# Kernel optimization log

Measured on AMD Instinct MI355X. Metric: run time of the kernel, lower is better.

The kernel has to match this reference:

```python
import jax, jax.numpy as jnp
import numpy as np

T_LEN, BATCH, IN_SIZE, HID = 512, 64, 1024, 1024
EPS = 1e-6


def layer_norm(x, alpha, beta, eps=EPS):
    # Matches torch: mean over last dim, UNBIASED variance (ddof=1)
    mu = jnp.mean(x, axis=-1, keepdims=True)
    var = jnp.var(x, axis=-1, keepdims=True, ddof=1)
    xn = (x - mu) / jnp.sqrt(var + eps)
    return alpha * xn + beta


def setup_inputs() -> dict:
    key = jax.random.key(0)
    ks = jax.random.split(key, 12)
    std = 1.0 / np.sqrt(HID)
    u = lambda k, shape: jax.random.uniform(k, shape, jnp.float32, -std, std)
    return {
        "x": jax.random.normal(ks[0], (T_LEN, BATCH, IN_SIZE), jnp.float32),
        "Wi": u(ks[1], (4 * HID, IN_SIZE)),
        "bi": u(ks[2], (4 * HID,)),
        "Wh": u(ks[3], (4 * HID, HID)),
        "bh": u(ks[4], (4 * HID,)),
        "g_i2h": u(ks[5], (4 * HID,)),
        "b_i2h": u(ks[6], (4 * HID,)),
        "g_h2h": u(ks[7], (4 * HID,)),
        "b_h2h": u(ks[8], (4 * HID,)),
        "g_cell": u(ks[9], (HID,)),
        "b_cell": u(ks[10], (HID,)),
    }


def reference(x, Wi, bi, Wh, bh, g_i2h, b_i2h, g_h2h, b_h2h, g_cell, b_cell):
    # Faithful to the source: h and c are NEVER updated inside the loop
    # (the original code omits h = h_t / c = c_t), so every timestep sees
    # the initial zero state -> fully parallel over time.
    T, B, _ = x.shape
    H = Wh.shape[1]
    h0 = jnp.zeros((B, H), x.dtype)
    c0 = jnp.zeros((B, H), x.dtype)

    i2h = layer_norm(jnp.einsum('tbi,gi->tbg', x, Wi) + bi, g_i2h, b_i2h)  # [T,B,4H]
    h2h = layer_norm(h0 @ Wh.T + bh, g_h2h, b_h2h)                          # [B,4H]
    preact = i2h + h2h                                                      # [T,B,4H]

    gates = jax.nn.sigmoid(preact[..., :3 * H])
    g_t = jnp.tanh(preact[..., 3 * H:])
    f_t = gates[..., H:2 * H]
    o_t = gates[..., 2 * H:3 * H]
    # i_t = gates[..., :H] is computed in the original but unused

    c_t = c0 * f_t + (1.0 - f_t) * g_t
    c_t = layer_norm(c_t, g_cell, b_cell)
    h_t = o_t * jnp.tanh(c_t)  # [T,B,H]

    return h_t, h_t[-1]
```

## Files before the change

### kernel.cpp

```cpp
#include <hip/hip_runtime.h>
#include <hip/hip_bf16.h>
#include <stdint.h>


#define MROWS 32768L
#define NCOLS 4096
#define KDIM  1024

typedef __bf16 bf16x8 __attribute__((ext_vector_type(8)));
typedef __bf16 bf16x4 __attribute__((ext_vector_type(4)));
typedef float  f32x4  __attribute__((ext_vector_type(4)));

__device__ float g_Cvec[4096];

__device__ __forceinline__ void gload16(char* lds, const char* g) {
  __builtin_amdgcn_global_load_lds(
      (const __attribute__((address_space(1))) char*)g,
      (__attribute__((address_space(3))) char*)lds, 16, 0, 0);
}

__device__ __forceinline__ void block_reduce2(float& a, float& b, float* red, int tid) {
#pragma unroll
  for (int m = 32; m > 0; m >>= 1) {
    a += __shfl_xor(a, m, 64);
    b += __shfl_xor(b, m, 64);
  }
  const int lane = tid & 63, wid = tid >> 6;
  if (lane == 0) { red[wid] = a; red[4 + wid] = b; }
  __syncthreads();
  a = red[0] + red[1] + red[2] + red[3];
  b = red[4] + red[5] + red[6] + red[7];
  __syncthreads();
}

__global__ __launch_bounds__(256) void cast_kernel(const float4* __restrict__ in,
                                                   bf16x4* __restrict__ out, int n4) {
  int i = blockIdx.x * 256 + threadIdx.x;
  const int stride = gridDim.x * 256;
  for (; i < n4; i += stride) {
    const float4 v = in[i];
    bf16x4 o = { (__bf16)v.x, (__bf16)v.y, (__bf16)v.z, (__bf16)v.w };
    out[i] = o;
  }
}

__global__ __launch_bounds__(256) void prep_kernel(const float* __restrict__ bh,
                                                   const float* __restrict__ b_i2h,
                                                   const float* __restrict__ g_h2h,
                                                   const float* __restrict__ b_h2h) {
  __shared__ float red[8];
  const int tid = threadIdx.x;
  float v[16];
  float s = 0.f, ss = 0.f;
#pragma unroll
  for (int u = 0; u < 16; ++u) {
    v[u] = bh[tid + u * 256];
    s += v[u]; ss += v[u] * v[u];
  }
  block_reduce2(s, ss, red, tid);
  const float mu  = s * (1.f / 4096.f);
  const float var = (ss - 4096.f * mu * mu) * (1.f / 4095.f);
  const float rs  = rsqrtf(var + 1e-6f);
#pragma unroll
  for (int u = 0; u < 16; ++u) {
    const int g = tid + u * 256;
    g_Cvec[g] = b_i2h[g] + g_h2h[g] * ((v[u] - mu) * rs) + b_h2h[g];
  }
}

__global__ __launch_bounds__(256) void gemm_kernel(const __bf16* __restrict__ A,
                                                   const __bf16* __restrict__ B,
                                                   __bf16* __restrict__ Y, long r0) {
  __shared__ __align__(16) __bf16 As[128 * 64];
  __shared__ __align__(16) __bf16 Bs[128 * 64];
  const int tid  = threadIdx.x;
  const int lane = tid & 63;
  const int wid  = tid >> 6;
  const int wm   = wid >> 1;
  const int wn   = wid & 1;
  const int bid  = blockIdx.x;
  const long m0  = (long)(bid >> 5) * 128;
  const long n0  = (long)(bid & 31) * 128;

  const int srow  = tid >> 3;
  const int sbyte = (tid & 7) << 4;
  const char* Ag = (const char*)(A + (r0 + m0) * KDIM) + (long)srow * 2048 + sbyte;
  const char* Bg = (const char*)(B + n0 * KDIM) + (long)srow * 2048 + sbyte;
  char* Al = (char*)As + tid * 16;
  char* Bl = (char*)Bs + tid * 16;

  f32x4 acc[4][4];
  const f32x4 z = {0.f, 0.f, 0.f, 0.f};
#pragma unroll
  for (int i = 0; i < 4; ++i)
#pragma unroll
    for (int j = 0; j < 4; ++j) acc[i][j] = z;

  const int fr = lane & 15;
  const int fk = (lane >> 4) << 3;
  const __bf16* ArdBase = &As[(wm * 64 + fr) * 64 + fk];
  const __bf16* BrdBase = &Bs[(wn * 64 + fr) * 64 + fk];

  for (int kt = 0; kt < KDIM / 64; ++kt) {
    const long koff = (long)kt * 128;
#pragma unroll
    for (int c = 0; c < 4; ++c) {
      gload16(Al + c * 4096, Ag + (long)c * 32 * 2048 + koff);
      gload16(Bl + c * 4096, Bg + (long)c * 32 * 2048 + koff);
    }
    __syncthreads();
#pragma unroll
    for (int s = 0; s < 2; ++s) {
      bf16x8 a[4], b[4];
#pragma unroll
      for (int i = 0; i < 4; ++i) a[i] = *(const bf16x8*)(ArdBase + i * 16 * 64 + s * 32);
#pragma unroll
      for (int j = 0; j < 4; ++j) b[j] = *(const bf16x8*)(BrdBase + j * 16 * 64 + s * 32);
#pragma unroll
      for (int i = 0; i < 4; ++i)
#pragma unroll
        for (int j = 0; j < 4; ++j)
          acc[i][j] = __builtin_amdgcn_mfma_f32_16x16x32_bf16(a[i], b[j], acc[i][j], 0, 0, 0);
    }
    __syncthreads();
  }

  const long orow0 = m0 + wm * 64 + ((lane >> 4) << 2);
  const long ocol0 = n0 + wn * 64 + fr;
#pragma unroll
  for (int i = 0; i < 4; ++i)
#pragma unroll
    for (int j = 0; j < 4; ++j)
#pragma unroll
      for (int r = 0; r < 4; ++r)
        Y[(orow0 + i * 16 + r) * NCOLS + ocol0 + j * 16] = (__bf16)acc[i][j][r];
}

__global__ __launch_bounds__(256) void pass2_kernel(const __bf16* __restrict__ Yw,
                                                    const float* __restrict__ bi,
                                                    const float* __restrict__ g_i2h,
                                                    const float* __restrict__ g_cell,
                                                    const float* __restrict__ b_cell,
                                                    float* __restrict__ out, long r0) {
  __shared__ float p0[4096];
  __shared__ float red[8];
  const int tid  = threadIdx.x;
  const long row = r0 + blockIdx.x;
  const bf16x8* yv = (const bf16x8*)(Yw + (long)blockIdx.x * NCOLS);

  float s = 0.f, ss = 0.f;
#pragma unroll
  for (int it = 0; it < 2; ++it) {
    const int ch = tid + it * 256;
    const bf16x8 v = yv[ch];
    const float4 b0 = ((const float4*)bi)[ch * 2];
    const float4 b1 = ((const float4*)bi)[ch * 2 + 1];
    float p[8];
    p[0] = (float)v[0] + b0.x;  p[1] = (float)v[1] + b0.y;
    p[2] = (float)v[2] + b0.z;  p[3] = (float)v[3] + b0.w;
    p[4] = (float)v[4] + b1.x;  p[5] = (float)v[5] + b1.y;
    p[6] = (float)v[6] + b1.z;  p[7] = (float)v[7] + b1.w;
#pragma unroll
    for (int u = 0; u < 8; ++u) {
      p0[ch * 8 + u] = p[u];
      s += p[u];
      ss += p[u] * p[u];
    }
  }
  block_reduce2(s, ss, red, tid);
  const float mu  = s * (1.f / 4096.f);
  const float var = (ss - 4096.f * mu * mu) * (1.f / 4095.f);
  const float rs  = rsqrtf(var + 1e-6f);

  float cc[4], oo[4];
  float s2 = 0.f, ss2 = 0.f;
#pragma unroll
  for (int u = 0; u < 4; ++u) {
    const int j = tid + u * 256;
    const float pf = g_i2h[1024 + j] * ((p0[1024 + j] - mu) * rs) + g_Cvec[1024 + j];
    const float po = g_i2h[2048 + j] * ((p0[2048 + j] - mu) * rs) + g_Cvec[2048 + j];
    const float pg = g_i2h[3072 + j] * ((p0[3072 + j] - mu) * rs) + g_Cvec[3072 + j];
    const float f  = 1.f / (1.f + __expf(-pf));
    oo[u] = 1.f / (1.f + __expf(-po));
    const float e2 = __expf(2.f * pg);
    const float gt = (e2 - 1.f) / (e2 + 1.f);
    cc[u] = (1.f - f) * gt;
    s2 += cc[u]; ss2 += cc[u] * cc[u];
  }
  block_reduce2(s2, ss2, red, tid);
  const float mu2  = s2 * (1.f / 1024.f);
  const float var2 = (ss2 - 1024.f * mu2 * mu2) * (1.f / 1023.f);
  const float rs2  = rsqrtf(var2 + 1e-6f);

  const long obase = row * 1024;
#pragma unroll
  for (int u = 0; u < 4; ++u) {
    const int j = tid + u * 256;
    const float cn = g_cell[j] * ((cc[u] - mu2) * rs2) + b_cell[j];
    const float e2 = __expf(2.f * cn);
    const float th = (e2 - 1.f) / (e2 + 1.f);
    const float h  = oo[u] * th;
    out[obase + j] = h;
    if (row >= MROWS - 64)
      out[MROWS * 1024 + ((row - (MROWS - 64)) << 10) + j] = h;
  }
}

extern "C" void kernel_launch(void* const* d_in, const int* in_sizes, int n_in,
                              void* d_out, int out_size, void* d_ws, size_t ws_size,
                              hipStream_t stream) {
  (void)in_sizes; (void)n_in; (void)out_size;
  const float* x      = (const float*)d_in[0];
  const float* Wi     = (const float*)d_in[1];
  const float* bi     = (const float*)d_in[2];
  const float* bh     = (const float*)d_in[4];
  const float* g_i2h  = (const float*)d_in[5];
  const float* b_i2h  = (const float*)d_in[6];
  const float* g_h2h  = (const float*)d_in[7];
  const float* b_h2h  = (const float*)d_in[8];
  const float* g_cell = (const float*)d_in[9];
  const float* b_cell = (const float*)d_in[10];
  float* out = (float*)d_out;

  __bf16* xb = (__bf16*)d_out;
  __bf16* wb = (__bf16*)((char*)d_out + 67108864);
  __bf16* y  = (__bf16*)d_ws;

  cast_kernel<<<2048, 256, 0, stream>>>((const float4*)x, (bf16x4*)xb, 33554432 / 4);
  cast_kernel<<<1024, 256, 0, stream>>>((const float4*)Wi, (bf16x4*)wb, 4194304 / 4);
  prep_kernel<<<1, 256, 0, stream>>>(bh, b_i2h, g_h2h, b_h2h);

  long max_rows = (long)(ws_size / (NCOLS * 2)) & ~127L;
  if (max_rows > MROWS) max_rows = MROWS;
  if (max_rows < 128)   max_rows = 128;
  for (long rbase = 0; rbase < MROWS; rbase += max_rows) {
    const long rows = (MROWS - rbase < max_rows) ? (MROWS - rbase) : max_rows;
    gemm_kernel<<<dim3((rows / 128) * 32), 256, 0, stream>>>(xb, wb, y, rbase);
    pass2_kernel<<<dim3(rows), 256, 0, stream>>>(y, bi, g_i2h, g_cell, b_cell, out, rbase);
  }
}
```

Measured before the change: 501.0 us.

## Rewrite GEMM with 256x256 tiles, double-buffered LDS pipeline and XCD-aware block mapping

New measurement: 513.4 us. +2.5%, slower.

```diff
diff --git a/kernel.cpp b/kernel.cpp
--- a/kernel.cpp
+++ b/kernel.cpp
@@ -68,72 +68,117 @@
   }
 }
 
-__global__ __launch_bounds__(256) void gemm_kernel(const __bf16* __restrict__ A,
-                                                   const __bf16* __restrict__ B,
-                                                   __bf16* __restrict__ Y, long r0) {
-  __shared__ __align__(16) __bf16 As[128 * 64];
-  __shared__ __align__(16) __bf16 Bs[128 * 64];
+
+#define PH_MID() do { asm volatile("" ::: "memory"); __builtin_amdgcn_s_barrier(); \
+    asm volatile("s_waitcnt lgkmcnt(0)" ::: "memory"); \
+    __builtin_amdgcn_sched_barrier(0); __builtin_amdgcn_s_setprio(1); } while (0)
+
+#define PH_END() do { __builtin_amdgcn_s_setprio(0); \
+    asm volatile("" ::: "memory"); __builtin_amdgcn_s_barrier(); } while (0)
+
+#define STG_A(s, h) { char* d_ = Al + (((s) & 1) << 15) + ((h) << 14); \
+    const char* g_ = Ag + (long)(h) * 262144 + (s) * 128; \
+    gload16(d_, g_); gload16(d_ + 8192, g_ + 131072); }
+
+#define STG_B(s, h) { char* d_ = Bl + (((s) & 1) << 15) + ((h) << 14); \
+    const char* g_ = Bg + (long)(h) * 262144 + (s) * 128; \
+    gload16(d_, g_); gload16(d_ + 8192, g_ + 131072); }
+
+#define RD_A(arr, c) { _Pragma("unroll") for (int mi_ = 0; mi_ < 4; ++mi_) { \
+    const char* p_ = Ahalf + (((c) * 64 + mi_ * 16 + fr) << 7); \
+    arr[mi_][0] = *(const bf16x8*)(p_ + cb0); \
+    arr[mi_][1] = *(const bf16x8*)(p_ + cb1); } }
+
+#define RD_B(g) { _Pragma("unroll") for (int nj_ = 0; nj_ < 2; ++nj_) { \
+    const char* p_ = Bhalf + ((brow0 + (g) * 32 + nj_ * 16 + fr) << 7); \
+    b[nj_][0] = *(const bf16x8*)(p_ + cb0); \
+    b[nj_][1] = *(const bf16x8*)(p_ + cb1); } }
+
+#define MM_Q(arr, c, g) { _Pragma("unroll") for (int mi_ = 0; mi_ < 4; ++mi_) { \
+    _Pragma("unroll") for (int nj_ = 0; nj_ < 2; ++nj_) { \
+      acc[(c)*4+mi_][(g)*2+nj_] = __builtin_amdgcn_mfma_f32_16x16x32_bf16( \
+          arr[mi_][0], b[nj_][0], acc[(c)*4+mi_][(g)*2+nj_], 0, 0, 0); \
+      acc[(c)*4+mi_][(g)*2+nj_] = __builtin_amdgcn_mfma_f32_16x16x32_bf16( \
+          arr[mi_][1], b[nj_][1], acc[(c)*4+mi_][(g)*2+nj_], 0, 0, 0); } } }
+
+__global__ __launch_bounds__(512, 2) void gemm_kernel(const __bf16* __restrict__ A,
+                                                      const __bf16* __restrict__ B,
+                                                      __bf16* __restrict__ Y, long r0) {
+  __shared__ __align__(16) __bf16 As[2 * 2 * 8192];
+  __shared__ __align__(16) __bf16 Bs[2 * 2 * 8192];
+
   const int tid  = threadIdx.x;
   const int lane = tid & 63;
   const int wid  = tid >> 6;
-  const int wm   = wid >> 1;
-  const int wn   = wid & 1;
-  const int bid  = blockIdx.x;
-  const long m0  = (long)(bid >> 5) * 128;
-  const long n0  = (long)(bid & 31) * 128;
-
-  const int srow  = tid >> 3;
-  const int sbyte = (tid & 7) << 4;
-  const char* Ag = (const char*)(A + (r0 + m0) * KDIM) + (long)srow * 2048 + sbyte;
-  const char* Bg = (const char*)(B + n0 * KDIM) + (long)srow * 2048 + sbyte;
+  const int wr   = wid >> 2;
+  const int wc   = wid & 3;
+
+  const int nwg = gridDim.x;
+  const int q8 = nwg >> 3, r8 = nwg & 7;
+  const int xcd = blockIdx.x & 7, rest = blockIdx.x >> 3;
+  const int wgid = (xcd < r8 ? xcd * (q8 + 1) : r8 * (q8 + 1) + (xcd - r8) * q8) + rest;
+  const long m0 = (long)(wgid >> 4) * 256;
+  const long n0 = (long)(wgid & 15) * 256;
+
+  const int scol = ((tid & 7) << 4) ^ (((tid >> 5) & 1) << 5);
+  const char* Ag = (const char*)(A + (r0 + m0) * KDIM) + (long)(tid >> 3) * 2048 + scol;
+  const char* Bg = (const char*)(B + n0 * KDIM) + (long)(tid >> 3) * 2048 + scol;
   char* Al = (char*)As + tid * 16;
   char* Bl = (char*)Bs + tid * 16;
 
-  f32x4 acc[4][4];
+  const int fr  = lane & 15;
+  const int cb0 = (((lane >> 4) << 4)) ^ ((fr & 4) << 3);
+  const int cb1 = (64 + ((lane >> 4) << 4)) ^ ((fr & 4) << 3);
+  const int brow0 = (wc & 1) << 6;
+
+  f32x4 acc[8][4];
   const f32x4 z = {0.f, 0.f, 0.f, 0.f};
 #pragma unroll
-  for (int i = 0; i < 4; ++i)
+  for (int i = 0; i < 8; ++i)
 #pragma unroll
     for (int j = 0; j < 4; ++j) acc[i][j] = z;
 
-  const int fr = lane & 15;
-  const int fk = (lane >> 4) << 3;
-  const __bf16* ArdBase = &As[(wm * 64 + fr) * 64 + fk];
-  const __bf16* BrdBase = &Bs[(wn * 64 + fr) * 64 + fk];
-
-  for (int kt = 0; kt < KDIM / 64; ++kt) {
-    const long koff = (long)kt * 128;
-#pragma unroll
-    for (int c = 0; c < 4; ++c) {
-      gload16(Al + c * 4096, Ag + (long)c * 32 * 2048 + koff);
-      gload16(Bl + c * 4096, Bg + (long)c * 32 * 2048 + koff);
-    }
-    __syncthreads();
-#pragma unroll
-    for (int s = 0; s < 2; ++s) {
-      bf16x8 a[4], b[4];
-#pragma unroll
-      for (int i = 0; i < 4; ++i) a[i] = *(const bf16x8*)(ArdBase + i * 16 * 64 + s * 32);
-#pragma unroll
-      for (int j = 0; j < 4; ++j) b[j] = *(const bf16x8*)(BrdBase + j * 16 * 64 + s * 32);
-#pragma unroll
-      for (int i = 0; i < 4; ++i)
-#pragma unroll
-        for (int j = 0; j < 4; ++j)
-          acc[i][j] = __builtin_amdgcn_mfma_f32_16x16x32_bf16(a[i], b[j], acc[i][j], 0, 0, 0);
-    }
-    __syncthreads();
-  }
-
-  const long orow0 = m0 + wm * 64 + ((lane >> 4) << 2);
-  const long ocol0 = n0 + wn * 64 + fr;
-#pragma unroll
-  for (int i = 0; i < 4; ++i)
-#pragma unroll
-    for (int j = 0; j < 4; ++j)
-#pragma unroll
-      for (int r = 0; r < 4; ++r)
-        Y[(orow0 + i * 16 + r) * NCOLS + ocol0 + j * 16] = (__bf16)acc[i][j][r];
+  STG_A(0, 0); STG_A(0, 1); STG_B(0, 0); STG_B(0, 1); STG_A(1, 0); STG_A(1, 1);
+  asm volatile("s_waitcnt vmcnt(4)" ::: "memory");
+  __builtin_amdgcn_s_barrier();
+
+  bf16x8 aa[4][2], ab[4][2], b[2][2];
+
+#pragma unroll 2
+  for (int t = 0; t < 16; ++t) {
+    const char* Ahalf = (const char*)As + ((t & 1) << 15) + (wr << 14);
+    const char* Bhalf = (const char*)Bs + ((t & 1) << 15) + ((wc >> 1) << 14);
+
+    RD_A(aa, 0); RD_B(0);
+    if (t + 1 < 16) STG_B(t + 1, 0);
+    PH_MID(); MM_Q(aa, 0, 0); PH_END();
+    RD_A(ab, 1);
+    if (t + 1 < 16) STG_B(t + 1, 1);
+    PH_MID(); MM_Q(ab, 1, 0); PH_END();
+    RD_B(1);
+    if (t + 2 < 16) STG_A(t + 2, 0);
+    PH_MID(); MM_Q(ab, 1, 1); PH_END();
+    if (t + 2 < 16) STG_A(t + 2, 1);
+    PH_MID(); MM_Q(aa, 0, 1);
+    __builtin_amdgcn_s_setprio(0);
+    if (t == 14)      { asm volatile("s_waitcnt vmcnt(0)" ::: "memory"); }
+    else if (t < 14)  { asm volatile("s_waitcnt vmcnt(4)" ::: "memory"); }
+    asm volatile("" ::: "memory");
+    __builtin_amdgcn_s_barrier();
+  }
+
+  const long mrow = m0 + wr * 128 + ((lane >> 4) << 2);
+  const long ncol = n0 + wc * 64 + fr;
+  __bf16* Yp = Y + mrow * NCOLS + ncol;
+#pragma unroll
+  for (int c = 0; c < 2; ++c)
+#pragma unroll
+    for (int mi = 0; mi < 4; ++mi)
+#pragma unroll
+      for (int nj = 0; nj < 4; ++nj)
+#pragma unroll
+        for (int r = 0; r < 4; ++r)
+          Yp[(long)(c * 64 + mi * 16 + r) * NCOLS + nj * 16] = (__bf16)acc[c * 4 + mi][nj][r];
 }
 
 __global__ __launch_bounds__(256) void pass2_kernel(const __bf16* __restrict__ Yw,
@@ -230,12 +275,12 @@
   cast_kernel<<<1024, 256, 0, stream>>>((const float4*)Wi, (bf16x4*)wb, 4194304 / 4);
   prep_kernel<<<1, 256, 0, stream>>>(bh, b_i2h, g_h2h, b_h2h);
 
-  long max_rows = (long)(ws_size / (NCOLS * 2)) & ~127L;
+  long max_rows = (long)(ws_size / (NCOLS * 2)) & ~255L;
   if (max_rows > MROWS) max_rows = MROWS;
-  if (max_rows < 128)   max_rows = 128;
+  if (max_rows < 256)   max_rows = 256;
   for (long rbase = 0; rbase < MROWS; rbase += max_rows) {
     const long rows = (MROWS - rbase < max_rows) ? (MROWS - rbase) : max_rows;
-    gemm_kernel<<<dim3((rows / 128) * 32), 256, 0, stream>>>(xb, wb, y, rbase);
+    gemm_kernel<<<dim3((rows / 256) * 16), 512, 0, stream>>>(xb, wb, y, rbase);
     pass2_kernel<<<dim3(rows), 256, 0, stream>>>(y, bi, g_i2h, g_cell, b_cell, out, rbase);
   }
 }
```
